# Optimization experiments

Measured on AMD Instinct MI355X. Metric: run time of the kernel, lower is better.

The kernel has to match this reference:

```python
import jax, jax.numpy as jnp
import numpy as np

N = 3072      # packed vision tokens (multiple of _BLOCK=128, so no padding needed)
D = 1280      # hidden_size
H = 16        # num_heads
K = 80        # head_dim = D // H
NSEG = 8      # number of packed images/segments


def setup_inputs() -> dict:
    key = jax.random.key(0)
    ks = jax.random.split(key, 8)
    hidden_ND = jax.random.normal(ks[0], (N, D), jnp.float32)
    inner = jnp.sort(jax.random.randint(ks[1], (NSEG - 1,), 1, N)).astype(jnp.int32)
    cu_seqlens = jnp.concatenate([
        jnp.zeros((1,), jnp.int32), inner, jnp.full((1,), N, jnp.int32)])
    theta = jax.random.uniform(ks[2], (N, K), jnp.float32, 0.0, 2.0 * np.pi)
    cos_NK = jnp.cos(theta)
    sin_NK = jnp.sin(theta)
    sd = 1.0 / np.sqrt(D)  # lecun_normal-ish scale
    qkv_w = jax.random.normal(ks[3], (D, 3 * D), jnp.float32) * sd
    qkv_b = jax.random.normal(ks[4], (3 * D,), jnp.float32) * 0.01
    proj_w = jax.random.normal(ks[5], (D, D), jnp.float32) * sd
    proj_b = jax.random.normal(ks[6], (D,), jnp.float32) * 0.01
    return {"hidden_ND": hidden_ND, "cu_seqlens": cu_seqlens,
            "cos_NK": cos_NK, "sin_NK": sin_NK,
            "qkv_w": qkv_w, "qkv_b": qkv_b,
            "proj_w": proj_w, "proj_b": proj_b}


def _rotate_half(x):
    x1, x2 = jnp.split(x, 2, axis=-1)
    return jnp.concatenate([-x2, x1], axis=-1)


def _apply_vision_rope(q_NHK, k_NHK, cos_NK, sin_NK):
    c = cos_NK[:, None, :]  # (N, 1, K) broadcast over heads
    s = sin_NK[:, None, :]
    q = q_NHK * c + _rotate_half(q_NHK) * s
    k = k_NHK * c + _rotate_half(k_NHK) * s
    return q, k


def reference(hidden_ND, cu_seqlens, cos_NK, sin_NK, qkv_w, qkv_b, proj_w, proj_b):
    n = hidden_ND.shape[0]
    scale = K ** (-0.5)
    qkv = (hidden_ND @ qkv_w + qkv_b).reshape(n, 3, H, K)
    q_NHK, k_NHK, v_NHK = qkv[:, 0], qkv[:, 1], qkv[:, 2]
    q_NHK, k_NHK = _apply_vision_rope(q_NHK, k_NHK, cos_NK, sin_NK)

    # segment-boundary mask: token i attends to [k_start[i], k_end[i])
    idx = jnp.arange(n)
    seg = jnp.searchsorted(cu_seqlens[1:], idx, side='right')
    nseg = cu_seqlens.shape[0]
    k_start = cu_seqlens[jnp.minimum(seg, nseg - 2)]
    k_end = cu_seqlens[jnp.minimum(seg + 1, nseg - 1)]
    mask = (idx[None, :] >= k_start[:, None]) & (idx[None, :] < k_end[:, None])  # (Nq, Nk)

    scores = jnp.einsum('nhk,mhk->hnm', q_NHK, k_NHK) * scale  # (H, N, N)
    scores = jnp.where(mask[None], scores, jnp.float32(-1e30))
    probs = jax.nn.softmax(scores, axis=-1)
    attn = jnp.einsum('hnm,mhk->nhk', probs, v_NHK)  # (N, H, K)
    out_ND = attn.reshape(n, H * K) @ proj_w + proj_b
    return out_ND
```

## Files before the change

kernel.cpp:

```cpp
#include <hip/hip_runtime.h>

#define NTOK 3072
#define DM   1280
#define NH   16
#define HD   80
#define HDS  96
#define KVB  64
#define NSEG 8
#define QKVC 3840

typedef __attribute__((ext_vector_type(4))) float  f32x4;
typedef __attribute__((ext_vector_type(8))) __bf16 bf16x8;
typedef __attribute__((ext_vector_type(8))) unsigned short ushort8;
typedef __attribute__((ext_vector_type(4))) unsigned short ushort4v;
typedef __attribute__((ext_vector_type(2))) unsigned int  u32x2;

static __device__ __forceinline__ unsigned short f2bf(float f){
  union{float f; unsigned int u;} v; v.f=f;
  unsigned int r = v.u + 0x7fffu + ((v.u>>16)&1u);
  return (unsigned short)(r>>16);
}
static __device__ __forceinline__ float bf2f(unsigned short u){
  union{unsigned int i; float f;} v; v.i = ((unsigned int)u)<<16; return v.f;
}
static __device__ __forceinline__ void gload_lds16(const void* g, void* l){
  __builtin_amdgcn_global_load_lds((const __attribute__((address_space(1))) void*)g,
                                   (__attribute__((address_space(3))) void*)l, 16, 0, 0);
}

__global__ void cast_f32_bf16(const float* __restrict__ src, unsigned short* __restrict__ dst, int n){
  int i = (blockIdx.x*256 + threadIdx.x)*4;
  if (i >= n) return;
  f32x4 v = *reinterpret_cast<const f32x4*>(&src[i]);
  ushort4v o;
  o[0]=f2bf(v[0]); o[1]=f2bf(v[1]); o[2]=f2bf(v[2]); o[3]=f2bf(v[3]);
  *reinterpret_cast<ushort4v*>(&dst[i]) = o;
}

__global__ void transpose_cast(const float* __restrict__ src, unsigned short* __restrict__ dst, int R, int C){
  __shared__ unsigned short tile[32][33];
  int c0 = blockIdx.x*32, r0 = blockIdx.y*32;
  int tx = threadIdx.x, ty = threadIdx.y;
  #pragma unroll
  for (int i=0;i<4;i++){
    int r = r0 + ty + i*8;
    tile[ty+i*8][tx] = f2bf(src[(size_t)r*C + c0 + tx]);
  }
  __syncthreads();
  #pragma unroll
  for (int i=0;i<4;i++){
    int c = c0 + ty + i*8;
    dst[(size_t)c*R + r0 + tx] = tile[tx][ty+i*8];
  }
}

__global__ void transpose_v(const unsigned short* __restrict__ qkv, unsigned short* __restrict__ Vt){
  __shared__ unsigned short tile[32][33];
  int n0 = blockIdx.x*32, d0 = blockIdx.y*32, h = blockIdx.z;
  int tx = threadIdx.x, ty = threadIdx.y;
  #pragma unroll
  for (int i=0;i<4;i++){
    int n = n0 + ty + i*8;
    int d = d0 + tx;
    tile[ty+i*8][tx] = (d < HD) ? qkv[(size_t)n*QKVC + 2*DM + h*HD + d] : (unsigned short)0;
  }
  __syncthreads();
  #pragma unroll
  for (int i=0;i<4;i++){
    int d = d0 + ty + i*8;
    if (d < HD) Vt[((size_t)h*HD + d)*NTOK + n0 + tx] = tile[tx][ty+i*8];
  }
}

template<int OUT_BF16>
__global__ __launch_bounds__(256) void gemm_bt(
    const unsigned short* __restrict__ A,
    const unsigned short* __restrict__ Bt,
    const float* __restrict__ bias,
    unsigned short* __restrict__ Cb,
    float* __restrict__ Cf,
    int M, int Ncol, int Kd, int nbn)
{
  __shared__ unsigned short As[2][128*32];
  __shared__ unsigned short Bs[2][128*32];
  const int tid  = threadIdx.x;
  const int lane = tid & 63, wave = tid >> 6;
  const int wr = wave >> 1, wc = wave & 1;
  const int cpx = gridDim.x >> 3;
  const int id  = (blockIdx.x & 7)*cpx + (blockIdx.x >> 3);
  const int bm = id / nbn, bn = id % nbn;
  const f32x4 vzero = {0.f,0.f,0.f,0.f};

  f32x4 acc[4][4];
  #pragma unroll
  for (int i=0;i<4;i++)
    #pragma unroll
    for (int j=0;j<4;j++) acc[i][j] = vzero;

  const int rsub = lane>>2;
  const int kc   = (lane&3)*8;
  const unsigned short* Ab = A  + (size_t)(bm*128 + wave*32 + rsub)*Kd + kc;
  const unsigned short* Bb = Bt + (size_t)(bn*128 + wave*32 + rsub)*Kd + kc;

  #pragma unroll
  for (int i=0;i<2;i++){
    gload_lds16(Ab + (size_t)i*16*Kd, &As[0][(wave*2+i)*512]);
    gload_lds16(Bb + (size_t)i*16*Kd, &Bs[0][(wave*2+i)*512]);
  }
  __syncthreads();

  int cur = 0;
  for (int k0=32; k0<Kd; k0+=32){
    #pragma unroll
    for (int i=0;i<2;i++){
      gload_lds16(Ab + (size_t)i*16*Kd + k0, &As[cur^1][(wave*2+i)*512]);
      gload_lds16(Bb + (size_t)i*16*Kd + k0, &Bs[cur^1][(wave*2+i)*512]);
    }
    bf16x8 a[4], b[4];
    #pragma unroll
    for (int mf=0; mf<4; mf++)
      a[mf] = *reinterpret_cast<const bf16x8*>(&As[cur][(wr*64 + mf*16 + (lane&15))*32 + ((lane>>4)<<3)]);
    #pragma unroll
    for (int nf=0; nf<4; nf++)
      b[nf] = *reinterpret_cast<const bf16x8*>(&Bs[cur][(wc*64 + nf*16 + (lane&15))*32 + ((lane>>4)<<3)]);
    #pragma unroll
    for (int mf=0; mf<4; mf++)
      #pragma unroll
      for (int nf=0; nf<4; nf++)
        acc[mf][nf] = __builtin_amdgcn_mfma_f32_16x16x32_bf16(a[mf], b[nf], acc[mf][nf], 0,0,0);
    __syncthreads();
    cur ^= 1;
  }
  {
    bf16x8 a[4], b[4];
    #pragma unroll
    for (int mf=0; mf<4; mf++)
      a[mf] = *reinterpret_cast<const bf16x8*>(&As[cur][(wr*64 + mf*16 + (lane&15))*32 + ((lane>>4)<<3)]);
    #pragma unroll
    for (int nf=0; nf<4; nf++)
      b[nf] = *reinterpret_cast<const bf16x8*>(&Bs[cur][(wc*64 + nf*16 + (lane&15))*32 + ((lane>>4)<<3)]);
    #pragma unroll
    for (int mf=0; mf<4; mf++)
      #pragma unroll
      for (int nf=0; nf<4; nf++)
        acc[mf][nf] = __builtin_amdgcn_mfma_f32_16x16x32_bf16(a[mf], b[nf], acc[mf][nf], 0,0,0);
  }

  const int crow0 = bm*128 + wr*64;
  const int ccol0 = bn*128 + wc*64;
  #pragma unroll
  for (int nf=0; nf<4; nf++){
    int col = ccol0 + nf*16 + (lane&15);
    float bv = bias[col];
    #pragma unroll
    for (int mf=0; mf<4; mf++){
      #pragma unroll
      for (int r=0;r<4;r++){
        int row = crow0 + mf*16 + ((lane>>4)<<2) + r;
        float v = acc[mf][nf][r] + bv;
        if (OUT_BF16) Cb[(size_t)row*Ncol + col] = f2bf(v);
        else          Cf[(size_t)row*Ncol + col] = v;
      }
    }
  }
}

__global__ void rope_repack(const unsigned short* __restrict__ qkv,
                            const float* __restrict__ cosNK, const float* __restrict__ sinNK,
                            unsigned short* __restrict__ Qr, unsigned short* __restrict__ Kr)
{
  int idx = blockIdx.x*256 + threadIdx.x;
  if (idx >= NH*NTOK*HDS) return;
  int k  = idx % HDS;
  int nh = idx / HDS;
  int n  = nh % NTOK;
  int h  = nh / NTOK;
  size_t dsti = (size_t)(h*NTOK + n)*HDS + k;
  if (k >= HD){ Qr[dsti]=0; Kr[dsti]=0; return; }
  float c = cosNK[n*HD + k], s = sinNK[n*HD + k];
  int   kp  = (k < 40) ? (k+40) : (k-40);
  float sgn = (k < 40) ? -1.f : 1.f;
  size_t base = (size_t)n*QKVC + h*HD;
  float q   = bf2f(qkv[base + k]);
  float qp  = bf2f(qkv[base + kp]);
  float kk  = bf2f(qkv[base + DM + k]);
  float kkp = bf2f(qkv[base + DM + kp]);
  Qr[dsti] = f2bf(q*c  + sgn*qp*s);
  Kr[dsti] = f2bf(kk*c + sgn*kkp*s);
}

#define ANB  ((NTOK/64)*NH)
__global__ __launch_bounds__(256) void attn_kernel(
    const unsigned short* __restrict__ Qr,
    const unsigned short* __restrict__ Kr,
    const unsigned short* __restrict__ Vt,
    const int* __restrict__ cu,
    unsigned short* __restrict__ attn_out)
{
  __shared__ unsigned short Ps[64*KVB];

  const int bx  = blockIdx.x;
  const int id  = (bx & 7)*(ANB/8) + (bx >> 3);
  const int h   = id / (NTOK/64);
  const int q0  = (id % (NTOK/64))*64;
  const int tid = threadIdx.x;
  const int lane = tid & 63, wave = tid >> 6;
  const int l16 = lane & 15, g16 = lane >> 4;
  const int qrow = q0 + wave*16 + l16;
  const f32x4 vzero = {0.f,0.f,0.f,0.f};

  int seg = 0, seg0 = 0, seg1 = 0;
  #pragma unroll
  for (int j=1;j<NSEG;j++){
    int c = cu[j];
    seg  += (c <= qrow)  ? 1 : 0;
    seg0 += (c <= q0)    ? 1 : 0;
    seg1 += (c <= q0+63) ? 1 : 0;
  }
  const int rst = cu[seg], ren = cu[seg+1];
  const int kmin = cu[seg0], kmax = cu[seg1+1];
  const int kt0 = kmin & ~(KVB-1);

  bf16x8 bq[3];
  {
    const unsigned short* qsrc = Qr + ((size_t)h*NTOK + qrow)*HDS;
    #pragma unroll
    for (int ds=0; ds<3; ds++)
      bq[ds] = *reinterpret_cast<const bf16x8*>(&qsrc[ds*32 + g16*8]);
  }

  f32x4 accO[5];
  #pragma unroll
  for (int i=0;i<5;i++) accO[i] = vzero;
  float m_r = -1e30f, l_r = 0.f;
  const float scale = 0.11180339887498948f;

  const int prow  = wave*16 + l16;
  char* const psb = (char*)Ps;
  const int pswz  = (prow & 7) << 4;

  for (int kt = kt0; kt < kmax; kt += KVB){
    ushort8 vreg[2][5];
    #pragma unroll
    for (int ks=0; ks<2; ks++)
      #pragma unroll
      for (int cf=0; cf<5; cf++)
        vreg[ks][cf] = *reinterpret_cast<const ushort8*>(
            &Vt[((size_t)h*HD + cf*16 + l16)*NTOK + kt + ks*32 + g16*8]);

    const unsigned short* ksrc = Kr + ((size_t)h*NTOK + kt)*HDS;
    f32x4 accST[4];
    #pragma unroll
    for (int i=0;i<4;i++) accST[i] = vzero;
    #pragma unroll
    for (int ds=0; ds<3; ds++){
      #pragma unroll
      for (int f=0; f<4; f++){
        bf16x8 ak = *reinterpret_cast<const bf16x8*>(&ksrc[(size_t)(f*16 + l16)*HDS + ds*32 + g16*8]);
        accST[f] = __builtin_amdgcn_mfma_f32_16x16x32_bf16(ak, bq[ds], accST[f], 0,0,0);
      }
    }

    float mx = -1e30f;
    #pragma unroll
    for (int f=0; f<4; f++){
      #pragma unroll
      for (int r=0; r<4; r++){
        int kcol = kt + f*16 + g16*4 + r;
        bool ok = (kcol >= rst) && (kcol < ren);
        float s = accST[f][r]*scale;
        accST[f][r] = ok ? s : -3e38f;
        mx = fmaxf(mx, accST[f][r]);
      }
    }
    mx = fmaxf(mx, __shfl_xor(mx, 16));
    mx = fmaxf(mx, __shfl_xor(mx, 32));
    const float mnew  = fmaxf(m_r, mx);
    const float alpha = __expf(m_r - mnew);
    m_r = mnew;
    float lsum = 0.f;
    #pragma unroll
    for (int f=0; f<4; f++){
      #pragma unroll
      for (int r=0; r<4; r++){
        float e = __expf(accST[f][r] - mnew);
        accST[f][r] = e;
        lsum += e;
      }
    }
    lsum += __shfl_xor(lsum, 16);
    lsum += __shfl_xor(lsum, 32);
    l_r = l_r*alpha + lsum;
    #pragma unroll
    for (int cf=0; cf<5; cf++) accO[cf] *= alpha;

    #pragma unroll
    for (int f=0; f<4; f++){
      u32x2 pk;
      pk[0] = (unsigned int)f2bf(accST[f][0]) | ((unsigned int)f2bf(accST[f][1]) << 16);
      pk[1] = (unsigned int)f2bf(accST[f][2]) | ((unsigned int)f2bf(accST[f][3]) << 16);
      *reinterpret_cast<u32x2*>(psb + ((prow*128 + f*32 + g16*8) ^ pswz)) = pk;
    }

    #pragma unroll
    for (int ks=0; ks<2; ks++){
      bf16x8 bp = *reinterpret_cast<const bf16x8*>(psb + ((prow*128 + ks*64 + g16*16) ^ pswz));
      #pragma unroll
      for (int cf=0; cf<5; cf++){
        bf16x8 av = __builtin_bit_cast(bf16x8, vreg[ks][cf]);
        accO[cf] = __builtin_amdgcn_mfma_f32_16x16x32_bf16(av, bp, accO[cf], 0,0,0);
      }
    }
  }

  const float inv = 1.f / l_r;
  #pragma unroll
  for (int cf=0; cf<5; cf++){
    ushort4v o;
    #pragma unroll
    for (int r=0;r<4;r++) o[r] = f2bf(accO[cf][r]*inv);
    *reinterpret_cast<ushort4v*>(&attn_out[(size_t)qrow*DM + h*HD + cf*16 + g16*4]) = o;
  }
}

extern "C" void kernel_launch(void* const* d_in, const int* in_sizes, int n_in,
                              void* d_out, int out_size, void* d_ws, size_t ws_size,
                              hipStream_t stream)
{
  const float* hidden = (const float*)d_in[0];
  const int*   cu     = (const int*)  d_in[1];
  const float* cosNK  = (const float*)d_in[2];
  const float* sinNK  = (const float*)d_in[3];
  const float* qkv_w  = (const float*)d_in[4];
  const float* qkv_b  = (const float*)d_in[5];
  const float* proj_w = (const float*)d_in[6];
  const float* proj_b = (const float*)d_in[7];
  float* out = (float*)d_out;

  char* w = (char*)d_ws;
  unsigned short* hid_bf  = (unsigned short*)w;  w += (size_t)NTOK*DM*2;
  unsigned short* qkvwT   = (unsigned short*)w;  w += (size_t)QKVC*DM*2;
  unsigned short* projwT  = (unsigned short*)w;  w += (size_t)DM*DM*2;
  unsigned short* qkv_bf  = (unsigned short*)w;  w += (size_t)NTOK*QKVC*2;
  unsigned short* Qr      = (unsigned short*)w;  w += (size_t)NH*NTOK*HDS*2;
  unsigned short* Kr      = (unsigned short*)w;  w += (size_t)NH*NTOK*HDS*2;
  unsigned short* Vt      = qkvwT;
  unsigned short* attn_bf = hid_bf;

  cast_f32_bf16<<<(NTOK*DM/4 + 255)/256, 256, 0, stream>>>(hidden, hid_bf, NTOK*DM);
  transpose_cast<<<dim3(QKVC/32, DM/32), dim3(32,8), 0, stream>>>(qkv_w, qkvwT, DM, QKVC);
  transpose_cast<<<dim3(DM/32,  DM/32), dim3(32,8), 0, stream>>>(proj_w, projwT, DM, DM);
  gemm_bt<1><<<dim3((NTOK/128)*(QKVC/128)), 256, 0, stream>>>(hid_bf, qkvwT, qkv_b, qkv_bf, nullptr, NTOK, QKVC, DM, QKVC/128);
  rope_repack<<<(NH*NTOK*HDS + 255)/256, 256, 0, stream>>>(qkv_bf, cosNK, sinNK, Qr, Kr);
  transpose_v<<<dim3(NTOK/32, 3, NH), dim3(32,8), 0, stream>>>(qkv_bf, Vt);
  attn_kernel<<<dim3(ANB), 256, 0, stream>>>(Qr, Kr, Vt, cu, attn_bf);
  gemm_bt<0><<<dim3((NTOK/128)*(DM/128)), 256, 0, stream>>>(attn_bf, projwT, proj_b, nullptr, out, NTOK, DM, DM, DM/128);
}
```

Baseline: 261.6 us.

## Split attention KV loop across two wave groups and merge softmax partials

The attention block grows to 512 threads: two groups of four waves each take alternating KV tiles for the same 64 query rows, and their partial outputs, maxima and sums are combined through shared memory at the end. Each wave now also limits its KV range to its own 16-row segment span instead of the whole block's span. The aim is more parallelism per query block and fewer wasted masked tiles. The cost is a larger shared memory footprint, a block-wide sync, an extra combine step, and possibly lower occupancy from the 512-thread launch bounds.

```diff
diff --git a/kernel.cpp b/kernel.cpp
--- a/kernel.cpp
+++ b/kernel.cpp
@@ -190,14 +190,15 @@
 }
 
 #define ANB  ((NTOK/64)*NH)
-__global__ __launch_bounds__(256) void attn_kernel(
+__global__ __launch_bounds__(512) void attn_kernel(
     const unsigned short* __restrict__ Qr,
     const unsigned short* __restrict__ Kr,
     const unsigned short* __restrict__ Vt,
     const int* __restrict__ cu,
     unsigned short* __restrict__ attn_out)
 {
-  __shared__ unsigned short Ps[64*KVB];
+  __shared__ unsigned short Ps[8*16*KVB];
+  __shared__ float Comb[4][64][23];
 
   const int bx  = blockIdx.x;
   const int id  = (bx & 7)*(ANB/8) + (bx >> 3);
@@ -205,21 +206,23 @@
   const int q0  = (id % (NTOK/64))*64;
   const int tid = threadIdx.x;
   const int lane = tid & 63, wave = tid >> 6;
+  const int qsub = wave & 3, half = wave >> 2;
   const int l16 = lane & 15, g16 = lane >> 4;
-  const int qrow = q0 + wave*16 + l16;
+  const int qrow = q0 + qsub*16 + l16;
   const f32x4 vzero = {0.f,0.f,0.f,0.f};
 
-  int seg = 0, seg0 = 0, seg1 = 0;
+  const int rowA = q0 + qsub*16, rowB = rowA + 15;
+  int seg = 0, sA = 0, sB = 0;
   #pragma unroll
   for (int j=1;j<NSEG;j++){
     int c = cu[j];
-    seg  += (c <= qrow)  ? 1 : 0;
-    seg0 += (c <= q0)    ? 1 : 0;
-    seg1 += (c <= q0+63) ? 1 : 0;
+    seg += (c <= qrow) ? 1 : 0;
+    sA  += (c <= rowA) ? 1 : 0;
+    sB  += (c <= rowB) ? 1 : 0;
   }
   const int rst = cu[seg], ren = cu[seg+1];
-  const int kmin = cu[seg0], kmax = cu[seg1+1];
-  const int kt0 = kmin & ~(KVB-1);
+  const int kminW = cu[sA], kmaxW = cu[sB+1];
+  const int kt0w = kminW & ~(KVB-1);
 
   bf16x8 bq[3];
   {
@@ -235,11 +238,10 @@
   float m_r = -1e30f, l_r = 0.f;
   const float scale = 0.11180339887498948f;
 
-  const int prow  = wave*16 + l16;
-  char* const psb = (char*)Ps;
-  const int pswz  = (prow & 7) << 4;
-
-  for (int kt = kt0; kt < kmax; kt += KVB){
+  char* const psb = (char*)Ps + wave*2048;
+  const int pswz  = (l16 & 7) << 4;
+
+  for (int kt = kt0w + half*KVB; kt < kmaxW; kt += 2*KVB){
     ushort8 vreg[2][5];
     #pragma unroll
     for (int ks=0; ks<2; ks++)
@@ -299,12 +301,12 @@
       u32x2 pk;
       pk[0] = (unsigned int)f2bf(accST[f][0]) | ((unsigned int)f2bf(accST[f][1]) << 16);
       pk[1] = (unsigned int)f2bf(accST[f][2]) | ((unsigned int)f2bf(accST[f][3]) << 16);
-      *reinterpret_cast<u32x2*>(psb + ((prow*128 + f*32 + g16*8) ^ pswz)) = pk;
+      *reinterpret_cast<u32x2*>(psb + ((l16*128 + f*32 + g16*8) ^ pswz)) = pk;
     }
 
     #pragma unroll
     for (int ks=0; ks<2; ks++){
-      bf16x8 bp = *reinterpret_cast<const bf16x8*>(psb + ((prow*128 + ks*64 + g16*16) ^ pswz));
+      bf16x8 bp = *reinterpret_cast<const bf16x8*>(psb + ((l16*128 + ks*64 + g16*16) ^ pswz));
       #pragma unroll
       for (int cf=0; cf<5; cf++){
         bf16x8 av = __builtin_bit_cast(bf16x8, vreg[ks][cf]);
@@ -313,13 +315,28 @@
     }
   }
 
-  const float inv = 1.f / l_r;
-  #pragma unroll
-  for (int cf=0; cf<5; cf++){
-    ushort4v o;
-    #pragma unroll
-    for (int r=0;r<4;r++) o[r] = f2bf(accO[cf][r]*inv);
-    *reinterpret_cast<ushort4v*>(&attn_out[(size_t)qrow*DM + h*HD + cf*16 + g16*4]) = o;
+  if (half == 1){
+    float* dst = &Comb[qsub][lane][0];
+    #pragma unroll
+    for (int cf=0; cf<5; cf++)
+      #pragma unroll
+      for (int r=0; r<4; r++) dst[cf*4+r] = accO[cf][r];
+    dst[20] = m_r; dst[21] = l_r;
+  }
+  __syncthreads();
+  if (half == 0){
+    const float* src = &Comb[qsub][lane][0];
+    const float m1 = src[20], l1 = src[21];
+    const float M  = fmaxf(m_r, m1);
+    const float a0 = __expf(m_r - M), a1 = __expf(m1 - M);
+    const float inv = 1.f / (l_r*a0 + l1*a1);
+    #pragma unroll
+    for (int cf=0; cf<5; cf++){
+      ushort4v o;
+      #pragma unroll
+      for (int r=0;r<4;r++) o[r] = f2bf((accO[cf][r]*a0 + src[cf*4+r]*a1)*inv);
+      *reinterpret_cast<ushort4v*>(&attn_out[(size_t)qrow*DM + h*HD + cf*16 + g16*4]) = o;
+    }
   }
 }
 
@@ -353,6 +370,6 @@
   gemm_bt<1><<<dim3((NTOK/128)*(QKVC/128)), 256, 0, stream>>>(hid_bf, qkvwT, qkv_b, qkv_bf, nullptr, NTOK, QKVC, DM, QKVC/128);
   rope_repack<<<(NH*NTOK*HDS + 255)/256, 256, 0, stream>>>(qkv_bf, cosNK, sinNK, Qr, Kr);
   transpose_v<<<dim3(NTOK/32, 3, NH), dim3(32,8), 0, stream>>>(qkv_bf, Vt);
-  attn_kernel<<<dim3(ANB), 256, 0, stream>>>(Qr, Kr, Vt, cu, attn_bf);
+  attn_kernel<<<dim3(ANB), 512, 0, stream>>>(Qr, Kr, Vt, cu, attn_bf);
   gemm_bt<0><<<dim3((NTOK/128)*(DM/128)), 256, 0, stream>>>(attn_bf, projwT, proj_b, nullptr, out, NTOK, DM, DM, DM/128);
 }
```

Result: slower. 276.4 us (+5.7%).
